# Optimization experiments

Measured on AMD Instinct MI355X. Metric: run time of the kernel, lower is better.

Reference implementation:

```python
import jax, jax.numpy as jnp
import numpy as np

EPS_SCALE = 1.0
EPS_MIN = 1e-08
SOLVER_ITER = 50


def _solve_qp_simplex(M, n_iter=SOLVER_ITER):
    # Frank-Wolfe on the simplex: min_{alpha in simplex} alpha^T M alpha
    B, K, _ = M.shape
    alpha0 = jnp.full((B, K), 1.0 / K, dtype=M.dtype)

    def body(i, alpha):
        grad = 2.0 * jnp.einsum('bkj,bj->bk', M, alpha)  # (B,K)
        idx = jnp.argmin(grad, axis=1)                    # (B,)
        s = jax.nn.one_hot(idx, K, dtype=alpha.dtype)     # vertex of simplex
        step = 2.0 / (i + 2.0)
        return (1.0 - step) * alpha + step * s

    return jax.lax.fori_loop(0, n_iter, body, alpha0)


def setup_inputs() -> dict:
    key = jax.random.key(0)
    k1, k2, k3 = jax.random.split(key, 3)
    B, K = 4096, 128
    scores = jax.random.normal(k1, (B, K), dtype=jnp.float32)
    C = jax.random.uniform(k2, (B, K, K), dtype=jnp.float32)
    targets = jax.random.randint(k3, (B,), 0, K)
    return {"scores": scores, "C": C, "targets": targets}


def reference(scores, C, targets):
    B, K = scores.shape
    # eps = off-diagonal mean of C per example, scaled and clamped
    eps = (jnp.sum(C, axis=(1, 2)) - jnp.trace(C, axis1=1, axis2=2)) / (K * (K - 1))
    eps = jnp.maximum(EPS_SCALE * eps, EPS_MIN)  # (B,)
    # pairwise exponent kernel: -(f_i + f_j + C_ij)/eps, stabilized by per-example max
    exponent = -(scores[:, :, None] + scores[:, None, :] + C) / eps[:, None, None]
    shift = jnp.max(exponent, axis=(1, 2), keepdims=True)  # (B,1,1)
    M = jnp.exp(exponent - shift)  # (B,K,K)
    # inner simplex solve is NOT differentiated through (implicit FY loss)
    alpha = jax.lax.stop_gradient(_solve_qp_simplex(M, SOLVER_ITER))  # (B,K)
    val = jnp.einsum('bi,bij,bj->b', alpha, M, alpha)  # (B,)
    conjugate = -eps * (jnp.log(val + 1e-12) + shift.reshape(-1))
    f_y = jnp.take_along_axis(scores, targets[:, None], axis=1)[:, 0]
    return jnp.mean(conjugate - f_y)
```

## Files before the change

kernel.cpp:

```cpp
#include <hip/hip_runtime.h>
#include <hip/hip_bf16.h>

#define K 128
#define NB 4096
#define FW_ITERS 50

template<int CTRL>
__device__ __forceinline__ float dpp_fmin(float v) {
    int s = __builtin_amdgcn_update_dpp(__float_as_int(v), __float_as_int(v), CTRL, 0xF, 0xF, false);
    return fminf(v, __int_as_float(s));
}
template<int CTRL>
__device__ __forceinline__ float dpp_fadd(float v) {
    int s = __builtin_amdgcn_update_dpp(__float_as_int(v), __float_as_int(v), CTRL, 0xF, 0xF, false);
    return v + __int_as_float(s);
}

__device__ __forceinline__ float wave_fmin_all(float v) {
    v = dpp_fmin<0xB1>(v);
    v = dpp_fmin<0x4E>(v);
    v = dpp_fmin<0x124>(v);
    v = dpp_fmin<0x128>(v);
#if __has_builtin(__builtin_amdgcn_permlane16_swap)
    {
        auto r = __builtin_amdgcn_permlane16_swap(__float_as_int(v), __float_as_int(v), false, false);
        v = fminf(__int_as_float(r[0]), __int_as_float(r[1]));
    }
#else
    v = fminf(v, __shfl_xor(v, 16, 64));
#endif
#if __has_builtin(__builtin_amdgcn_permlane32_swap)
    {
        auto r = __builtin_amdgcn_permlane32_swap(__float_as_int(v), __float_as_int(v), false, false);
        v = fminf(__int_as_float(r[0]), __int_as_float(r[1]));
    }
#else
    v = fminf(v, __shfl_xor(v, 32, 64));
#endif
    return v;
}

__device__ __forceinline__ float half_sum32(float v) {
    v = dpp_fadd<0xB1>(v);
    v = dpp_fadd<0x4E>(v);
    v = dpp_fadd<0x124>(v);
    v = dpp_fadd<0x128>(v);
#if __has_builtin(__builtin_amdgcn_permlane16_swap)
    {
        auto r = __builtin_amdgcn_permlane16_swap(__float_as_int(v), __float_as_int(v), false, false);
        v = __int_as_float(r[0]) + __int_as_float(r[1]);
    }
#else
    v = v + __shfl_xor(v, 16, 64);
#endif
    return v;
}

__device__ __forceinline__ unsigned short bf16_bits(float f) {
    __hip_bfloat16 h = __float2bfloat16(f);
    return *reinterpret_cast<unsigned short*>(&h);
}

__device__ __forceinline__ int swz(int col) {
    return ((col >> 2) + ((col & 3) << 3)) & 31;
}

__global__ __launch_bounds__(256, 4) void cacis_main(
    const float* __restrict__ scores,
    const float* __restrict__ C,
    const int* __restrict__ targets,
    float* __restrict__ out_partial)
{
    __shared__ unsigned int Mw[K * 64];
    __shared__ __align__(16) float s_lds[K];
    __shared__ __align__(16) float grow[K];
    __shared__ __align__(16) float alpha[K];
    __shared__ float red[4][4];

    const int b = blockIdx.x;
    const int tid = threadIdx.x;
    const int w = tid >> 6;
    const int lane = tid & 63;

    if (b < 1024) {
        const int stag = (b >> 8) & 3;
        for (int i = 0; i < stag * 4; ++i) __builtin_amdgcn_s_sleep(32);
    }

    if (tid < K) s_lds[tid] = scores[b * K + tid];
    __syncthreads();

    const float* Cb = C + (size_t)b * (K * K);
    const int cb = 4 * (tid & 31);
    float4 c[16];
    float sc[4];
    {
        float4 s4 = *reinterpret_cast<const float4*>(&s_lds[cb]);
        sc[0] = s4.x; sc[1] = s4.y; sc[2] = s4.z; sc[3] = s4.w;
    }

    #pragma unroll
    for (int j = 0; j < 16; ++j)
        c[j] = *reinterpret_cast<const float4*>(Cb + 4 * tid + 1024 * j);

    float sumC = 0.f, trace = 0.f, minv = 1e30f;
    #pragma unroll
    for (int j = 0; j < 16; ++j) {
        const int row = 8 * j + (tid >> 5);
        const float sr = s_lds[row];
        float4 v = c[j];
        sumC += (v.x + v.y) + (v.z + v.w);
        const int d = row - cb;
        if (d >= 0 && d < 4)
            trace += (d == 0) ? v.x : (d == 1) ? v.y : (d == 2) ? v.z : v.w;
        float t0 = sr + sc[0] + v.x;
        float t1 = sr + sc[1] + v.y;
        float t2 = sr + sc[2] + v.z;
        float t3 = sr + sc[3] + v.w;
        c[j] = make_float4(t0, t1, t2, t3);
        minv = fminf(minv, fminf(fminf(t0, t1), fminf(t2, t3)));
    }

    #pragma unroll
    for (int m = 1; m < 64; m <<= 1) {
        sumC  += __shfl_xor(sumC, m, 64);
        trace += __shfl_xor(trace, m, 64);
        minv   = fminf(minv, __shfl_xor(minv, m, 64));
    }
    if (lane == 0) { red[w][0] = sumC; red[w][1] = trace; red[w][2] = minv; }
    __syncthreads();
    sumC  = (red[0][0] + red[1][0]) + (red[2][0] + red[3][0]);
    trace = (red[0][1] + red[1][1]) + (red[2][1] + red[3][1]);
    minv  = fminf(fminf(red[0][2], red[1][2]), fminf(red[2][2], red[3][2]));

    float eps = fmaxf((sumC - trace) * (1.0f / (float)(K * (K - 1))), 1e-8f);
    const float inv_eps = 1.0f / eps;

    #pragma unroll
    for (int j = 0; j < 16; ++j) {
        const int row = 8 * j + (tid >> 5);
        float4 t = c[j];
        float m0 = __expf((minv - t.x) * inv_eps);
        float m1 = __expf((minv - t.y) * inv_eps);
        float m2 = __expf((minv - t.z) * inv_eps);
        float m3 = __expf((minv - t.w) * inv_eps);
        const int r = row >> 1, hh = row & 1;
        ((unsigned short*)&Mw[((cb + 0) << 6) + (r ^ swz(cb + 0))])[hh] = bf16_bits(m0);
        ((unsigned short*)&Mw[((cb + 1) << 6) + (r ^ swz(cb + 1))])[hh] = bf16_bits(m1);
        ((unsigned short*)&Mw[((cb + 2) << 6) + (r ^ swz(cb + 2))])[hh] = bf16_bits(m2);
        ((unsigned short*)&Mw[((cb + 3) << 6) + (r ^ swz(cb + 3))])[hh] = bf16_bits(m3);
        float rs = half_sum32((m0 + m1) + (m2 + m3));
        if ((lane & 31) == 0) grow[row] = rs * (1.0f / (float)K);
    }
    __syncthreads();

    if (w == 0) {
        const int l = lane;
        float g0 = grow[2 * l], g1 = grow[2 * l + 1];
        float a0 = 1.0f / K, a1 = 1.0f / K;
        #pragma unroll 1
        for (int it = 0; it < FW_ITERS; ++it) {
            const float v = wave_fmin_all(fminf(g0, g1));
            unsigned long long b0 = __ballot(g0 == v);
            unsigned long long b1 = __ballot(g1 == v);
            int i0 = b0 ? 2 * (int)__builtin_ctzll(b0)     : 0x7fffffff;
            int i1 = b1 ? 2 * (int)__builtin_ctzll(b1) + 1 : 0x7fffffff;
            const int idx = min(i0, i1);

            const float step = 2.0f / (float)(it + 2);
            const float om = 1.0f - step;
            a0 *= om; a1 *= om;
            if (2 * l == idx)     a0 += step;
            if (2 * l + 1 == idx) a1 += step;
            unsigned uw = Mw[(idx << 6) + (l ^ swz(idx))];
            g0 = om * g0 + step * __uint_as_float(uw << 16);
            g1 = om * g1 + step * __uint_as_float(uw & 0xffff0000u);
        }
        alpha[2 * l]     = a0;
        alpha[2 * l + 1] = a1;
    }
    __syncthreads();

    {
        const int col = tid >> 1, rh = tid & 1;
        const int cb6 = col << 6, sw = swz(col);
        const float ac = alpha[col];
        float acc = 0.f;
        #pragma unroll
        for (int k = 0; k < 32; ++k) {
            const int r = rh * 32 + k;
            unsigned u = Mw[cb6 + (r ^ sw)];
            float2 ap = *reinterpret_cast<const float2*>(&alpha[2 * r]);
            acc += ap.x * __uint_as_float(u << 16) + ap.y * __uint_as_float(u & 0xffff0000u);
        }
        float valp = acc * ac;
        #pragma unroll
        for (int m = 1; m < 64; m <<= 1) valp += __shfl_xor(valp, m, 64);
        if (lane == 0) red[w][0] = valp;
    }
    __syncthreads();
    if (tid == 0) {
        const float val = (red[0][0] + red[1][0]) + (red[2][0] + red[3][0]);
        const float conj = -eps * logf(val + 1e-12f) + minv;
        const int tgt = targets[b];
        out_partial[b] = conj - s_lds[tgt];
    }
}

__global__ __launch_bounds__(256) void cacis_reduce(
    const float* __restrict__ part, float* __restrict__ out)
{
    __shared__ float red[4];
    const int tid = threadIdx.x;
    float acc = 0.f;
    for (int i = tid; i < NB; i += 256) acc += part[i];
    #pragma unroll
    for (int m = 1; m < 64; m <<= 1) acc += __shfl_xor(acc, m, 64);
    if ((tid & 63) == 0) red[tid >> 6] = acc;
    __syncthreads();
    if (tid == 0) out[0] = ((red[0] + red[1]) + (red[2] + red[3])) * (1.0f / (float)NB);
}

extern "C" void kernel_launch(void* const* d_in, const int* in_sizes, int n_in,
                              void* d_out, int out_size, void* d_ws, size_t ws_size,
                              hipStream_t stream) {
    const float* scores  = (const float*)d_in[0];
    const float* C       = (const float*)d_in[1];
    const int*   targets = (const int*)d_in[2];
    float* out  = (float*)d_out;
    float* part = (float*)d_ws;

    cacis_main<<<NB, 256, 0, stream>>>(scores, C, targets, part);
    cacis_reduce<<<1, 256, 0, stream>>>(part, out);
}
```

Before: 97.32 us.

## Process four examples per block and prefetch next example's C during Frank-Wolfe

Each block now loops over four examples. It issues global loads of the next example's C tile and scores into registers before the serial single-wave Frank-Wolfe solve, so memory latency overlaps with that solve. The start-up sleep staggering is removed and __syncthreads is replaced by a lighter LDS-wait barrier. The trade-off is a quarter as many blocks (1024), which may leave CUs underfilled with 4 blocks per CU. Results also carry over in registers between loop iterations, which may raise register pressure.

```diff
diff --git a/kernel.cpp b/kernel.cpp
--- a/kernel.cpp
+++ b/kernel.cpp
@@ -3,6 +3,8 @@
 
 #define K 128
 #define NB 4096
+#define EPB 4
+#define NBLK (NB / EPB)
 #define FW_ITERS 50
 
 template<int CTRL>
@@ -63,6 +65,12 @@
 
 __device__ __forceinline__ int swz(int col) {
     return ((col >> 2) + ((col & 3) << 3)) & 31;
+}
+
+__device__ __forceinline__ void barrier_lds() {
+    asm volatile("s_waitcnt lgkmcnt(0)" ::: "memory");
+    __builtin_amdgcn_s_barrier();
+    asm volatile("" ::: "memory");
 }
 
 __global__ __launch_bounds__(256, 4) void cacis_main(
@@ -81,129 +89,145 @@
     const int tid = threadIdx.x;
     const int w = tid >> 6;
     const int lane = tid & 63;
-
-    if (b < 1024) {
-        const int stag = (b >> 8) & 3;
-        for (int i = 0; i < stag * 4; ++i) __builtin_amdgcn_s_sleep(32);
-    }
-
-    if (tid < K) s_lds[tid] = scores[b * K + tid];
-    __syncthreads();
-
-    const float* Cb = C + (size_t)b * (K * K);
     const int cb = 4 * (tid & 31);
+
     float4 c[16];
-    float sc[4];
-    {
-        float4 s4 = *reinterpret_cast<const float4*>(&s_lds[cb]);
-        sc[0] = s4.x; sc[1] = s4.y; sc[2] = s4.z; sc[3] = s4.w;
-    }
-
-    #pragma unroll
-    for (int j = 0; j < 16; ++j)
-        c[j] = *reinterpret_cast<const float4*>(Cb + 4 * tid + 1024 * j);
-
-    float sumC = 0.f, trace = 0.f, minv = 1e30f;
-    #pragma unroll
-    for (int j = 0; j < 16; ++j) {
-        const int row = 8 * j + (tid >> 5);
-        const float sr = s_lds[row];
-        float4 v = c[j];
-        sumC += (v.x + v.y) + (v.z + v.w);
-        const int d = row - cb;
-        if (d >= 0 && d < 4)
-            trace += (d == 0) ? v.x : (d == 1) ? v.y : (d == 2) ? v.z : v.w;
-        float t0 = sr + sc[0] + v.x;
-        float t1 = sr + sc[1] + v.y;
-        float t2 = sr + sc[2] + v.z;
-        float t3 = sr + sc[3] + v.w;
-        c[j] = make_float4(t0, t1, t2, t3);
-        minv = fminf(minv, fminf(fminf(t0, t1), fminf(t2, t3)));
-    }
-
-    #pragma unroll
-    for (int m = 1; m < 64; m <<= 1) {
-        sumC  += __shfl_xor(sumC, m, 64);
-        trace += __shfl_xor(trace, m, 64);
-        minv   = fminf(minv, __shfl_xor(minv, m, 64));
-    }
-    if (lane == 0) { red[w][0] = sumC; red[w][1] = trace; red[w][2] = minv; }
-    __syncthreads();
-    sumC  = (red[0][0] + red[1][0]) + (red[2][0] + red[3][0]);
-    trace = (red[0][1] + red[1][1]) + (red[2][1] + red[3][1]);
-    minv  = fminf(fminf(red[0][2], red[1][2]), fminf(red[2][2], red[3][2]));
-
-    float eps = fmaxf((sumC - trace) * (1.0f / (float)(K * (K - 1))), 1e-8f);
-    const float inv_eps = 1.0f / eps;
-
-    #pragma unroll
-    for (int j = 0; j < 16; ++j) {
-        const int row = 8 * j + (tid >> 5);
-        float4 t = c[j];
-        float m0 = __expf((minv - t.x) * inv_eps);
-        float m1 = __expf((minv - t.y) * inv_eps);
-        float m2 = __expf((minv - t.z) * inv_eps);
-        float m3 = __expf((minv - t.w) * inv_eps);
-        const int r = row >> 1, hh = row & 1;
-        ((unsigned short*)&Mw[((cb + 0) << 6) + (r ^ swz(cb + 0))])[hh] = bf16_bits(m0);
-        ((unsigned short*)&Mw[((cb + 1) << 6) + (r ^ swz(cb + 1))])[hh] = bf16_bits(m1);
-        ((unsigned short*)&Mw[((cb + 2) << 6) + (r ^ swz(cb + 2))])[hh] = bf16_bits(m2);
-        ((unsigned short*)&Mw[((cb + 3) << 6) + (r ^ swz(cb + 3))])[hh] = bf16_bits(m3);
-        float rs = half_sum32((m0 + m1) + (m2 + m3));
-        if ((lane & 31) == 0) grow[row] = rs * (1.0f / (float)K);
-    }
-    __syncthreads();
-
-    if (w == 0) {
-        const int l = lane;
-        float g0 = grow[2 * l], g1 = grow[2 * l + 1];
-        float a0 = 1.0f / K, a1 = 1.0f / K;
-        #pragma unroll 1
-        for (int it = 0; it < FW_ITERS; ++it) {
-            const float v = wave_fmin_all(fminf(g0, g1));
-            unsigned long long b0 = __ballot(g0 == v);
-            unsigned long long b1 = __ballot(g1 == v);
-            int i0 = b0 ? 2 * (int)__builtin_ctzll(b0)     : 0x7fffffff;
-            int i1 = b1 ? 2 * (int)__builtin_ctzll(b1) + 1 : 0x7fffffff;
-            const int idx = min(i0, i1);
-
-            const float step = 2.0f / (float)(it + 2);
-            const float om = 1.0f - step;
-            a0 *= om; a1 *= om;
-            if (2 * l == idx)     a0 += step;
-            if (2 * l + 1 == idx) a1 += step;
-            unsigned uw = Mw[(idx << 6) + (l ^ swz(idx))];
-            g0 = om * g0 + step * __uint_as_float(uw << 16);
-            g1 = om * g1 + step * __uint_as_float(uw & 0xffff0000u);
-        }
-        alpha[2 * l]     = a0;
-        alpha[2 * l + 1] = a1;
-    }
-    __syncthreads();
-
-    {
-        const int col = tid >> 1, rh = tid & 1;
-        const int cb6 = col << 6, sw = swz(col);
-        const float ac = alpha[col];
-        float acc = 0.f;
-        #pragma unroll
-        for (int k = 0; k < 32; ++k) {
-            const int r = rh * 32 + k;
-            unsigned u = Mw[cb6 + (r ^ sw)];
-            float2 ap = *reinterpret_cast<const float2*>(&alpha[2 * r]);
-            acc += ap.x * __uint_as_float(u << 16) + ap.y * __uint_as_float(u & 0xffff0000u);
-        }
-        float valp = acc * ac;
-        #pragma unroll
-        for (int m = 1; m < 64; m <<= 1) valp += __shfl_xor(valp, m, 64);
-        if (lane == 0) red[w][0] = valp;
-    }
-    __syncthreads();
-    if (tid == 0) {
-        const float val = (red[0][0] + red[1][0]) + (red[2][0] + red[3][0]);
-        const float conj = -eps * logf(val + 1e-12f) + minv;
-        const int tgt = targets[b];
-        out_partial[b] = conj - s_lds[tgt];
+    float sreg;
+    int4 tgts;
+    {
+        const float* Cb = C + (size_t)(b * EPB) * (K * K);
+        #pragma unroll
+        for (int j = 0; j < 16; ++j)
+            c[j] = *reinterpret_cast<const float4*>(Cb + 4 * tid + 1024 * j);
+        if (tid < K) sreg = scores[(b * EPB) * K + tid];
+        if (tid == 0) tgts = *reinterpret_cast<const int4*>(&targets[b * EPB]);
+    }
+
+    #pragma unroll 1
+    for (int ee = 0; ee < EPB; ++ee) {
+        const int ex = b * EPB + ee;
+
+        if (tid < K) s_lds[tid] = sreg;
+        barrier_lds();
+
+        float f_y = 0.f;
+        if (tid == 0) {
+            const int tgt = (ee == 0) ? tgts.x : (ee == 1) ? tgts.y : (ee == 2) ? tgts.z : tgts.w;
+            f_y = s_lds[tgt];
+        }
+
+        float sc0, sc1, sc2, sc3;
+        {
+            float4 s4 = *reinterpret_cast<const float4*>(&s_lds[cb]);
+            sc0 = s4.x; sc1 = s4.y; sc2 = s4.z; sc3 = s4.w;
+        }
+        float sumC = 0.f, trace = 0.f, minv = 1e30f;
+        #pragma unroll
+        for (int j = 0; j < 16; ++j) {
+            const int row = 8 * j + (tid >> 5);
+            const float sr = s_lds[row];
+            float4 v = c[j];
+            sumC += (v.x + v.y) + (v.z + v.w);
+            const int d = row - cb;
+            if (d >= 0 && d < 4)
+                trace += (d == 0) ? v.x : (d == 1) ? v.y : (d == 2) ? v.z : v.w;
+            float t0 = sr + sc0 + v.x;
+            float t1 = sr + sc1 + v.y;
+            float t2 = sr + sc2 + v.z;
+            float t3 = sr + sc3 + v.w;
+            c[j] = make_float4(t0, t1, t2, t3);
+            minv = fminf(minv, fminf(fminf(t0, t1), fminf(t2, t3)));
+        }
+        #pragma unroll
+        for (int m = 1; m < 64; m <<= 1) {
+            sumC  += __shfl_xor(sumC, m, 64);
+            trace += __shfl_xor(trace, m, 64);
+            minv   = fminf(minv, __shfl_xor(minv, m, 64));
+        }
+        if (lane == 0) { red[w][0] = sumC; red[w][1] = trace; red[w][2] = minv; }
+        barrier_lds();
+        sumC  = (red[0][0] + red[1][0]) + (red[2][0] + red[3][0]);
+        trace = (red[0][1] + red[1][1]) + (red[2][1] + red[3][1]);
+        minv  = fminf(fminf(red[0][2], red[1][2]), fminf(red[2][2], red[3][2]));
+
+        const float eps = fmaxf((sumC - trace) * (1.0f / (float)(K * (K - 1))), 1e-8f);
+        const float inv_eps = 1.0f / eps;
+
+        #pragma unroll
+        for (int j = 0; j < 16; ++j) {
+            const int row = 8 * j + (tid >> 5);
+            float4 t = c[j];
+            float m0 = __expf((minv - t.x) * inv_eps);
+            float m1 = __expf((minv - t.y) * inv_eps);
+            float m2 = __expf((minv - t.z) * inv_eps);
+            float m3 = __expf((minv - t.w) * inv_eps);
+            const int r = row >> 1, hh = row & 1;
+            ((unsigned short*)&Mw[((cb + 0) << 6) + (r ^ swz(cb + 0))])[hh] = bf16_bits(m0);
+            ((unsigned short*)&Mw[((cb + 1) << 6) + (r ^ swz(cb + 1))])[hh] = bf16_bits(m1);
+            ((unsigned short*)&Mw[((cb + 2) << 6) + (r ^ swz(cb + 2))])[hh] = bf16_bits(m2);
+            ((unsigned short*)&Mw[((cb + 3) << 6) + (r ^ swz(cb + 3))])[hh] = bf16_bits(m3);
+            float rs = half_sum32((m0 + m1) + (m2 + m3));
+            if ((lane & 31) == 0) grow[row] = rs * (1.0f / (float)K);
+        }
+
+        if (ee + 1 < EPB) {
+            const float* Cb_n = C + (size_t)(ex + 1) * (K * K);
+            #pragma unroll
+            for (int j = 0; j < 16; ++j)
+                c[j] = *reinterpret_cast<const float4*>(Cb_n + 4 * tid + 1024 * j);
+            if (tid < K) sreg = scores[(ex + 1) * K + tid];
+        }
+        barrier_lds();
+
+        if (w == 0) {
+            const int l = lane;
+            float g0 = grow[2 * l], g1 = grow[2 * l + 1];
+            float a0 = 1.0f / K, a1 = 1.0f / K;
+            #pragma unroll 1
+            for (int it = 0; it < FW_ITERS; ++it) {
+                const float v = wave_fmin_all(fminf(g0, g1));
+                unsigned long long b0 = __ballot(g0 == v);
+                unsigned long long b1 = __ballot(g1 == v);
+                int i0 = b0 ? 2 * (int)__builtin_ctzll(b0)     : 0x7fffffff;
+                int i1 = b1 ? 2 * (int)__builtin_ctzll(b1) + 1 : 0x7fffffff;
+                const int idx = min(i0, i1);
+
+                const float step = 2.0f / (float)(it + 2);
+                const float om = 1.0f - step;
+                a0 *= om; a1 *= om;
+                if (2 * l == idx)     a0 += step;
+                if (2 * l + 1 == idx) a1 += step;
+                unsigned uw = Mw[(idx << 6) + (l ^ swz(idx))];
+                g0 = om * g0 + step * __uint_as_float(uw << 16);
+                g1 = om * g1 + step * __uint_as_float(uw & 0xffff0000u);
+            }
+            alpha[2 * l]     = a0;
+            alpha[2 * l + 1] = a1;
+        }
+        barrier_lds();
+
+        {
+            const int col = tid >> 1, rh = tid & 1;
+            const int cb6 = col << 6, sw = swz(col);
+            const float ac = alpha[col];
+            float acc = 0.f;
+            #pragma unroll
+            for (int k = 0; k < 32; ++k) {
+                const int r = rh * 32 + k;
+                unsigned u = Mw[cb6 + (r ^ sw)];
+                float2 ap = *reinterpret_cast<const float2*>(&alpha[2 * r]);
+                acc += ap.x * __uint_as_float(u << 16) + ap.y * __uint_as_float(u & 0xffff0000u);
+            }
+            float valp = acc * ac;
+            #pragma unroll
+            for (int m = 1; m < 64; m <<= 1) valp += __shfl_xor(valp, m, 64);
+            if (lane == 0) red[w][0] = valp;
+        }
+        barrier_lds();
+        if (tid == 0) {
+            const float val = (red[0][0] + red[1][0]) + (red[2][0] + red[3][0]);
+            out_partial[ex] = -eps * logf(val + 1e-12f) + minv - f_y;
+        }
     }
 }
 
@@ -230,6 +254,6 @@
     float* out  = (float*)d_out;
     float* part = (float*)d_ws;
 
-    cacis_main<<<NB, 256, 0, stream>>>(scores, C, targets, part);
+    cacis_main<<<NBLK, 256, 0, stream>>>(scores, C, targets, part);
     cacis_reduce<<<1, 256, 0, stream>>>(part, out);
 }
```

Result: slower. 220.1 us (+126.2%).

## Process examples per wave with register prefetch of next C and grad-based quadratic

Applied to the files above, without the earlier changes.

Restructures the kernel so each wave independently handles four consecutive examples with its own LDS M buffer, removing block-wide syncs. It prefetches the next example's C tile into registers before running the serial Frank-Wolfe loop, so the global loads can overlap that loop. The final alpha^T M alpha is computed from the tracked gradient (alpha·g), which drops the separate matvec pass. Each thread now holds 64 float4 registers, which raises register pressure and lowers occupancy, with only 512 blocks of 128 threads. The initial sleep-based stagger is removed.

```diff
diff --git a/kernel.cpp b/kernel.cpp
--- a/kernel.cpp
+++ b/kernel.cpp
@@ -3,6 +3,9 @@
 
 #define K 128
 #define NB 4096
+#define EPW 4
+#define WPB 2
+#define NBLK (NB / (EPW * WPB))
 #define FW_ITERS 50
 
 template<int CTRL>
@@ -65,98 +68,99 @@
     return ((col >> 2) + ((col & 3) << 3)) & 31;
 }
 
-__global__ __launch_bounds__(256, 4) void cacis_main(
+__global__ __launch_bounds__(WPB * 64, 1) void cacis_main(
     const float* __restrict__ scores,
     const float* __restrict__ C,
     const int* __restrict__ targets,
     float* __restrict__ out_partial)
 {
-    __shared__ unsigned int Mw[K * 64];
-    __shared__ __align__(16) float s_lds[K];
-    __shared__ __align__(16) float grow[K];
-    __shared__ __align__(16) float alpha[K];
-    __shared__ float red[4][4];
-
-    const int b = blockIdx.x;
+    __shared__ unsigned int Mw[WPB][K * 64];
+    __shared__ __align__(16) float s_l[WPB][K];
+    __shared__ __align__(16) float grow[WPB][K];
+
     const int tid = threadIdx.x;
     const int w = tid >> 6;
-    const int lane = tid & 63;
-
-    if (b < 1024) {
-        const int stag = (b >> 8) & 3;
-        for (int i = 0; i < stag * 4; ++i) __builtin_amdgcn_s_sleep(32);
-    }
-
-    if (tid < K) s_lds[tid] = scores[b * K + tid];
-    __syncthreads();
-
-    const float* Cb = C + (size_t)b * (K * K);
-    const int cb = 4 * (tid & 31);
-    float4 c[16];
-    float sc[4];
-    {
-        float4 s4 = *reinterpret_cast<const float4*>(&s_lds[cb]);
-        sc[0] = s4.x; sc[1] = s4.y; sc[2] = s4.z; sc[3] = s4.w;
-    }
-
-    #pragma unroll
-    for (int j = 0; j < 16; ++j)
-        c[j] = *reinterpret_cast<const float4*>(Cb + 4 * tid + 1024 * j);
-
-    float sumC = 0.f, trace = 0.f, minv = 1e30f;
-    #pragma unroll
-    for (int j = 0; j < 16; ++j) {
-        const int row = 8 * j + (tid >> 5);
-        const float sr = s_lds[row];
-        float4 v = c[j];
-        sumC += (v.x + v.y) + (v.z + v.w);
-        const int d = row - cb;
-        if (d >= 0 && d < 4)
-            trace += (d == 0) ? v.x : (d == 1) ? v.y : (d == 2) ? v.z : v.w;
-        float t0 = sr + sc[0] + v.x;
-        float t1 = sr + sc[1] + v.y;
-        float t2 = sr + sc[2] + v.z;
-        float t3 = sr + sc[3] + v.w;
-        c[j] = make_float4(t0, t1, t2, t3);
-        minv = fminf(minv, fminf(fminf(t0, t1), fminf(t2, t3)));
-    }
-
-    #pragma unroll
-    for (int m = 1; m < 64; m <<= 1) {
-        sumC  += __shfl_xor(sumC, m, 64);
-        trace += __shfl_xor(trace, m, 64);
-        minv   = fminf(minv, __shfl_xor(minv, m, 64));
-    }
-    if (lane == 0) { red[w][0] = sumC; red[w][1] = trace; red[w][2] = minv; }
-    __syncthreads();
-    sumC  = (red[0][0] + red[1][0]) + (red[2][0] + red[3][0]);
-    trace = (red[0][1] + red[1][1]) + (red[2][1] + red[3][1]);
-    minv  = fminf(fminf(red[0][2], red[1][2]), fminf(red[2][2], red[3][2]));
-
-    float eps = fmaxf((sumC - trace) * (1.0f / (float)(K * (K - 1))), 1e-8f);
-    const float inv_eps = 1.0f / eps;
-
-    #pragma unroll
-    for (int j = 0; j < 16; ++j) {
-        const int row = 8 * j + (tid >> 5);
-        float4 t = c[j];
-        float m0 = __expf((minv - t.x) * inv_eps);
-        float m1 = __expf((minv - t.y) * inv_eps);
-        float m2 = __expf((minv - t.z) * inv_eps);
-        float m3 = __expf((minv - t.w) * inv_eps);
-        const int r = row >> 1, hh = row & 1;
-        ((unsigned short*)&Mw[((cb + 0) << 6) + (r ^ swz(cb + 0))])[hh] = bf16_bits(m0);
-        ((unsigned short*)&Mw[((cb + 1) << 6) + (r ^ swz(cb + 1))])[hh] = bf16_bits(m1);
-        ((unsigned short*)&Mw[((cb + 2) << 6) + (r ^ swz(cb + 2))])[hh] = bf16_bits(m2);
-        ((unsigned short*)&Mw[((cb + 3) << 6) + (r ^ swz(cb + 3))])[hh] = bf16_bits(m3);
-        float rs = half_sum32((m0 + m1) + (m2 + m3));
-        if ((lane & 31) == 0) grow[row] = rs * (1.0f / (float)K);
-    }
-    __syncthreads();
-
-    if (w == 0) {
-        const int l = lane;
-        float g0 = grow[2 * l], g1 = grow[2 * l + 1];
+    const int l = tid & 63;
+    const int half = l >> 5;
+    const int cb = 4 * (l & 31);
+    const int exbase = blockIdx.x * (EPW * WPB) + w * EPW;
+
+    float4 c[64];
+    {
+        const float* Cb = C + (size_t)exbase * (K * K);
+        #pragma unroll
+        for (int j = 0; j < 64; ++j)
+            c[j] = *reinterpret_cast<const float4*>(Cb + 4 * l + 256 * j);
+        s_l[w][l]      = scores[exbase * K + l];
+        s_l[w][l + 64] = scores[exbase * K + 64 + l];
+    }
+
+    #pragma unroll 1
+    for (int q = 0; q < EPW; ++q) {
+        const int ex = exbase + q;
+        const int tgt = targets[ex];
+        const float f_y = s_l[w][tgt];
+
+        float sc0, sc1, sc2, sc3;
+        {
+            float4 s4 = *reinterpret_cast<const float4*>(&s_l[w][cb]);
+            sc0 = s4.x; sc1 = s4.y; sc2 = s4.z; sc3 = s4.w;
+        }
+        float sumC = 0.f, trace = 0.f, minv = 1e30f;
+        #pragma unroll
+        for (int j = 0; j < 64; ++j) {
+            const int row = 2 * j + half;
+            const float sr = s_l[w][row];
+            float4 v = c[j];
+            sumC += (v.x + v.y) + (v.z + v.w);
+            const int d = row - cb;
+            if (d >= 0 && d < 4)
+                trace += (d == 0) ? v.x : (d == 1) ? v.y : (d == 2) ? v.z : v.w;
+            float t0 = sr + sc0 + v.x;
+            float t1 = sr + sc1 + v.y;
+            float t2 = sr + sc2 + v.z;
+            float t3 = sr + sc3 + v.w;
+            c[j] = make_float4(t0, t1, t2, t3);
+            minv = fminf(minv, fminf(fminf(t0, t1), fminf(t2, t3)));
+        }
+        #pragma unroll
+        for (int m = 1; m < 64; m <<= 1) {
+            sumC  += __shfl_xor(sumC, m, 64);
+            trace += __shfl_xor(trace, m, 64);
+            minv   = fminf(minv, __shfl_xor(minv, m, 64));
+        }
+        const float eps = fmaxf((sumC - trace) * (1.0f / (float)(K * (K - 1))), 1e-8f);
+        const float inv_eps = 1.0f / eps;
+
+        #pragma unroll
+        for (int j = 0; j < 64; ++j) {
+            float4 t = c[j];
+            float m0 = __expf((minv - t.x) * inv_eps);
+            float m1 = __expf((minv - t.y) * inv_eps);
+            float m2 = __expf((minv - t.z) * inv_eps);
+            float m3 = __expf((minv - t.w) * inv_eps);
+            ((unsigned short*)&Mw[w][((cb + 0) << 6) + (j ^ swz(cb + 0))])[half] = bf16_bits(m0);
+            ((unsigned short*)&Mw[w][((cb + 1) << 6) + (j ^ swz(cb + 1))])[half] = bf16_bits(m1);
+            ((unsigned short*)&Mw[w][((cb + 2) << 6) + (j ^ swz(cb + 2))])[half] = bf16_bits(m2);
+            ((unsigned short*)&Mw[w][((cb + 3) << 6) + (j ^ swz(cb + 3))])[half] = bf16_bits(m3);
+            float rs = half_sum32((m0 + m1) + (m2 + m3));
+            if ((l & 31) == 0) grow[w][2 * j + half] = rs * (1.0f / (float)K);
+        }
+
+        if (q + 1 < EPW) {
+            const float* Cb_n = C + (size_t)(ex + 1) * (K * K);
+            #pragma unroll
+            for (int j = 0; j < 64; ++j)
+                c[j] = *reinterpret_cast<const float4*>(Cb_n + 4 * l + 256 * j);
+            s_l[w][l]      = scores[(ex + 1) * K + l];
+            s_l[w][l + 64] = scores[(ex + 1) * K + 64 + l];
+        }
+
+        float g0, g1;
+        {
+            float2 g = *reinterpret_cast<const float2*>(&grow[w][2 * l]);
+            g0 = g.x; g1 = g.y;
+        }
         float a0 = 1.0f / K, a1 = 1.0f / K;
         #pragma unroll 1
         for (int it = 0; it < FW_ITERS; ++it) {
@@ -172,38 +176,17 @@
             a0 *= om; a1 *= om;
             if (2 * l == idx)     a0 += step;
             if (2 * l + 1 == idx) a1 += step;
-            unsigned uw = Mw[(idx << 6) + (l ^ swz(idx))];
+            unsigned uw = Mw[w][(idx << 6) + (l ^ swz(idx))];
             g0 = om * g0 + step * __uint_as_float(uw << 16);
             g1 = om * g1 + step * __uint_as_float(uw & 0xffff0000u);
         }
-        alpha[2 * l]     = a0;
-        alpha[2 * l + 1] = a1;
-    }
-    __syncthreads();
-
-    {
-        const int col = tid >> 1, rh = tid & 1;
-        const int cb6 = col << 6, sw = swz(col);
-        const float ac = alpha[col];
-        float acc = 0.f;
-        #pragma unroll
-        for (int k = 0; k < 32; ++k) {
-            const int r = rh * 32 + k;
-            unsigned u = Mw[cb6 + (r ^ sw)];
-            float2 ap = *reinterpret_cast<const float2*>(&alpha[2 * r]);
-            acc += ap.x * __uint_as_float(u << 16) + ap.y * __uint_as_float(u & 0xffff0000u);
-        }
-        float valp = acc * ac;
+
+        float valp = a0 * g0 + a1 * g1;
         #pragma unroll
         for (int m = 1; m < 64; m <<= 1) valp += __shfl_xor(valp, m, 64);
-        if (lane == 0) red[w][0] = valp;
-    }
-    __syncthreads();
-    if (tid == 0) {
-        const float val = (red[0][0] + red[1][0]) + (red[2][0] + red[3][0]);
-        const float conj = -eps * logf(val + 1e-12f) + minv;
-        const int tgt = targets[b];
-        out_partial[b] = conj - s_lds[tgt];
+        if (l == 0) {
+            out_partial[ex] = -eps * logf(valp + 1e-12f) + minv - f_y;
+        }
     }
 }
 
@@ -230,6 +213,6 @@
     float* out  = (float*)d_out;
     float* part = (float*)d_ws;
 
-    cacis_main<<<NB, 256, 0, stream>>>(scores, C, targets, part);
+    cacis_main<<<NBLK, WPB * 64, 0, stream>>>(scores, C, targets, part);
     cacis_reduce<<<1, 256, 0, stream>>>(part, out);
 }
```

New measurement: 223.3 us. +129.4%, slower.
